# Optimization experiments

Hardware: AMD Instinct MI355X
Metric: run time of the kernel (lower is better)

The kernel has to match this reference:

```python
import jax, jax.numpy as jnp
import numpy as np

H = 128          # num_hidden
B = 512          # number of graphs (segments)
N0, N1, N2 = 500_000, 500_000, 250_000  # nodes per rank
EPS = 1e-5       # LayerNorm eps (torch default)


def setup_inputs() -> dict:
    key = jax.random.key(0)
    ks = jax.random.split(key, 24)
    s = 0.02
    inp = {
        "h0": jax.random.normal(ks[0], (N0, H), jnp.float32),
        "h1": jax.random.normal(ks[1], (N1, H), jnp.float32),
        "h2": jax.random.normal(ks[2], (N2, H), jnp.float32),
        "b0": jnp.sort(jax.random.randint(ks[3], (N0,), 0, B, jnp.int32)),
        "b1": jnp.sort(jax.random.randint(ks[4], (N1,), 0, B, jnp.int32)),
        "b2": jnp.sort(jax.random.randint(ks[5], (N2,), 0, B, jnp.int32)),
        "Wg0": jax.random.normal(ks[6], (H, 1), jnp.float32) * s,
        "bg0": jnp.zeros((1,), jnp.float32),
        "Wg1": jax.random.normal(ks[7], (H, 1), jnp.float32) * s,
        "bg1": jnp.zeros((1,), jnp.float32),
        "Wg2": jax.random.normal(ks[8], (H, 1), jnp.float32) * s,
        "bg2": jnp.zeros((1,), jnp.float32),
        "Wp0": jax.random.normal(ks[9], (4 * H, H), jnp.float32) * s,
        "bp0": jnp.zeros((H,), jnp.float32),
        "Wp1": jax.random.normal(ks[10], (4 * H, H), jnp.float32) * s,
        "bp1": jnp.zeros((H,), jnp.float32),
        "Wp2": jax.random.normal(ks[11], (4 * H, H), jnp.float32) * s,
        "bp2": jnp.zeros((H,), jnp.float32),
        "gamma": jnp.ones((3 * H,), jnp.float32),
        "beta": jnp.zeros((3 * H,), jnp.float32),
        "W1": jax.random.normal(ks[12], (3 * H, H), jnp.float32) * s,
        "b1f": jnp.zeros((H,), jnp.float32),
        "W2": jax.random.normal(ks[13], (H, 1), jnp.float32) * s,
        "b2f": jnp.zeros((1,), jnp.float32),
    }
    return inp


def _rank_vec(h, b, Wg, bg, Wp, bp):
    # gated multi-aggregation pooling over segments b -> [B, 4H] -> Linear -> [B, H]
    g = jax.nn.sigmoid(h @ Wg + bg)                      # [N, 1]
    sum_p = jax.ops.segment_sum(h, b, num_segments=B)    # [B, H]
    cnt = jax.ops.segment_sum(jnp.ones((h.shape[0], 1), h.dtype), b, num_segments=B)
    mean_p = sum_p / jnp.maximum(cnt, 1.0)
    max_p = jax.ops.segment_max(h, b, num_segments=B)
    max_p = jnp.where(cnt > 0, max_p, 0.0)               # guard empty segments
    gsum_p = jax.ops.segment_sum(g * h, b, num_segments=B)
    agg = jnp.concatenate([sum_p, mean_p, max_p, gsum_p], axis=1)  # [B, 4H]
    return agg @ Wp + bp


def reference(h0, h1, h2, b0, b1, b2,
              Wg0, bg0, Wg1, bg1, Wg2, bg2,
              Wp0, bp0, Wp1, bp1, Wp2, bp2,
              gamma, beta, W1, b1f, W2, b2f):
    r0 = _rank_vec(h0, b0, Wg0, bg0, Wp0, bp0)
    r1 = _rank_vec(h1, b1, Wg1, bg1, Wp1, bp1)
    r2 = _rank_vec(h2, b2, Wg2, bg2, Wp2, bp2)
    state = jnp.concatenate([r0, r1, r2], axis=1)        # [B, 3H]
    mu = jnp.mean(state, axis=-1, keepdims=True)
    var = jnp.mean(jnp.square(state - mu), axis=-1, keepdims=True)
    xn = (state - mu) * jax.lax.rsqrt(var + EPS) * gamma + beta
    x = jax.nn.silu(xn)
    x = jax.nn.silu(x @ W1 + b1f)
    out = x @ W2 + b2f                                   # [B, 1]
    return out[:, 0] if out.shape[-1] == 1 else out
```

## Files before the change

kernel.cpp:

```cpp
#include <hip/hip_runtime.h>
#include <hip/hip_bf16.h>
#include <math.h>

constexpr int H  = 128;
constexpr int B  = 512;
constexpr int CHUNK = 64;
constexpr int RANK_STRIDE = 3 * B * H + B;
constexpr int TOTAL_WS    = 3 * RANK_STRIDE;

__device__ __forceinline__ float atomicMaxF(float* addr, float val) {
  if (val >= 0.f) {
    return __int_as_float(atomicMax((int*)addr, __float_as_int(val)));
  } else {
    return __uint_as_float(atomicMin((unsigned int*)addr, __float_as_uint(val)));
  }
}

__global__ __launch_bounds__(256) void init_ws_kernel(float* ws) {
  int i = blockIdx.x * blockDim.x + threadIdx.x;
  if (i >= TOTAL_WS) return;
  int o = i % RANK_STRIDE;
  bool ismax = (o >= 2 * B * H) && (o < 3 * B * H);
  ws[i] = ismax ? __int_as_float(0xFF800000) : 0.0f;
}

__global__ __launch_bounds__(256) void rank_kernel(
    const float* __restrict__ h, const int* __restrict__ b,
    const float* __restrict__ Wg, const float* __restrict__ bg,
    float* __restrict__ sumb, float* __restrict__ gsumb,
    float* __restrict__ maxb, float* __restrict__ cntb, int N)
{
  const int lane = threadIdx.x & 63;
  const int wave = threadIdx.x >> 6;
  const long long gw = (long long)blockIdx.x * 4 + wave;
  const int row0 = (int)(gw * CHUNK);
  if (row0 >= N) return;
  const int row1 = min(N, row0 + CHUNK);

  const float2 wg = ((const float2*)Wg)[lane];
  const float bgv = bg[0];

  float s0 = 0.f, s1 = 0.f, g0 = 0.f, g1 = 0.f;
  float m0 = -INFINITY, m1 = -INFINITY;
  int cnt = 0;
  int cur = b[row0];

  for (int r = row0; r < row1; ++r) {
    const int seg = b[r];
    const float2 hv = ((const float2*)h)[(long long)r * 64 + lane];
    if (seg != cur) {
      const int base = cur * H + 2 * lane;
      atomicAdd(sumb + base,     s0); atomicAdd(sumb + base + 1,  s1);
      atomicAdd(gsumb + base,    g0); atomicAdd(gsumb + base + 1, g1);
      atomicMaxF(maxb + base,    m0); atomicMaxF(maxb + base + 1, m1);
      if (lane == 0) atomicAdd(cntb + cur, (float)cnt);
      s0 = s1 = g0 = g1 = 0.f; m0 = m1 = -INFINITY; cnt = 0; cur = seg;
    }
    float part = hv.x * wg.x + hv.y * wg.y;
    part += __shfl_xor(part, 1);
    part += __shfl_xor(part, 2);
    part += __shfl_xor(part, 4);
    part += __shfl_xor(part, 8);
    part += __shfl_xor(part, 16);
    part += __shfl_xor(part, 32);
    const float gate = 1.0f / (1.0f + __expf(-(part + bgv)));

    s0 += hv.x;                 s1 += hv.y;
    g0 = fmaf(gate, hv.x, g0);  g1 = fmaf(gate, hv.y, g1);
    m0 = fmaxf(m0, hv.x);       m1 = fmaxf(m1, hv.y);
    ++cnt;
  }
  if (cnt > 0) {
    const int base = cur * H + 2 * lane;
    atomicAdd(sumb + base,     s0); atomicAdd(sumb + base + 1,  s1);
    atomicAdd(gsumb + base,    g0); atomicAdd(gsumb + base + 1, g1);
    atomicMaxF(maxb + base,    m0); atomicMaxF(maxb + base + 1, m1);
    if (lane == 0) atomicAdd(cntb + cur, (float)cnt);
  }
}

__device__ __forceinline__ float siluf(float x) {
  return x / (1.0f + __expf(-x));
}

__global__ __launch_bounds__(128) void finalize_kernel(
    const float* __restrict__ ws,
    const float* __restrict__ Wp0, const float* __restrict__ bp0,
    const float* __restrict__ Wp1, const float* __restrict__ bp1,
    const float* __restrict__ Wp2, const float* __restrict__ bp2,
    const float* __restrict__ gamma, const float* __restrict__ beta,
    const float* __restrict__ W1, const float* __restrict__ b1f,
    const float* __restrict__ W2, const float* __restrict__ b2f,
    float* __restrict__ out)
{
  __shared__ float aggL[4][4 * H];
  __shared__ float state[4][3 * H];
  __shared__ float red[8];

  const int j = threadIdx.x;
  const int lane = j & 63;
  const int wv = j >> 6;
  const int gbase = blockIdx.x * 4;

  const float* Wp[3] = {Wp0, Wp1, Wp2};
  const float* bp[3] = {bp0, bp1, bp2};

  for (int k = 0; k < 3; ++k) {
    const float* sumb  = ws + k * RANK_STRIDE;
    const float* gsumb = sumb + B * H;
    const float* maxb  = sumb + 2 * B * H;
    const float* cntb  = sumb + 3 * B * H;

    for (int g = 0; g < 4; ++g) {
      const int bidx = gbase + g;
      const float c  = cntb[bidx];
      const float cm = fmaxf(c, 1.0f);
      const float sv = sumb[bidx * H + j];
      const float mv = maxb[bidx * H + j];
      const float gv = gsumb[bidx * H + j];
      aggL[g][j]         = sv;
      aggL[g][H + j]     = sv / cm;
      aggL[g][2 * H + j] = (c > 0.f) ? mv : 0.f;
      aggL[g][3 * H + j] = gv;
    }
    __syncthreads();

    const float bpv = bp[k][j];
    float r0 = bpv, r1 = bpv, r2 = bpv, r3 = bpv;
    const float* W = Wp[k];
    for (int i = 0; i < 4 * H; ++i) {
      const float w = W[i * H + j];
      r0 = fmaf(aggL[0][i], w, r0);
      r1 = fmaf(aggL[1][i], w, r1);
      r2 = fmaf(aggL[2][i], w, r2);
      r3 = fmaf(aggL[3][i], w, r3);
    }
    state[0][k * H + j] = r0;
    state[1][k * H + j] = r1;
    state[2][k * H + j] = r2;
    state[3][k * H + j] = r3;
    __syncthreads();
  }

  for (int g = 0; g < 4; ++g) {
    const float v0 = state[g][j];
    const float v1 = state[g][H + j];
    const float v2 = state[g][2 * H + j];
    float ps = v0 + v1 + v2;
    float pq = v0 * v0 + v1 * v1 + v2 * v2;
    for (int m = 1; m < 64; m <<= 1) {
      ps += __shfl_xor(ps, m);
      pq += __shfl_xor(pq, m);
    }
    if (lane == 0) { red[wv * 2] = ps; red[wv * 2 + 1] = pq; }
    __syncthreads();
    const float ts = red[0] + red[2];
    const float tq = red[1] + red[3];
    const float mu  = ts * (1.0f / 384.0f);
    const float var = tq * (1.0f / 384.0f) - mu * mu;
    const float inv = rsqrtf(var + 1e-5f);
    float x0 = (v0 - mu) * inv * gamma[j]         + beta[j];
    float x1 = (v1 - mu) * inv * gamma[H + j]     + beta[H + j];
    float x2 = (v2 - mu) * inv * gamma[2 * H + j] + beta[2 * H + j];
    state[g][j]         = siluf(x0);
    state[g][H + j]     = siluf(x1);
    state[g][2 * H + j] = siluf(x2);
    __syncthreads();
  }

  const float b1v = b1f[j];
  float a0 = b1v, a1 = b1v, a2 = b1v, a3 = b1v;
  for (int i = 0; i < 3 * H; ++i) {
    const float w = W1[i * H + j];
    a0 = fmaf(state[0][i], w, a0);
    a1 = fmaf(state[1][i], w, a1);
    a2 = fmaf(state[2][i], w, a2);
    a3 = fmaf(state[3][i], w, a3);
  }
  a0 = siluf(a0); a1 = siluf(a1); a2 = siluf(a2); a3 = siluf(a3);

  const float w2 = W2[j];
  float p0 = a0 * w2, p1 = a1 * w2, p2 = a2 * w2, p3 = a3 * w2;
  for (int m = 1; m < 64; m <<= 1) {
    p0 += __shfl_xor(p0, m);
    p1 += __shfl_xor(p1, m);
    p2 += __shfl_xor(p2, m);
    p3 += __shfl_xor(p3, m);
  }
  __syncthreads();
  if (lane == 0) {
    red[wv * 4 + 0] = p0; red[wv * 4 + 1] = p1;
    red[wv * 4 + 2] = p2; red[wv * 4 + 3] = p3;
  }
  __syncthreads();
  if (j < 4) out[gbase + j] = red[j] + red[4 + j] + b2f[0];
}

extern "C" void kernel_launch(void* const* d_in, const int* in_sizes, int n_in,
                              void* d_out, int out_size, void* d_ws, size_t ws_size,
                              hipStream_t stream) {
  const float* h0  = (const float*)d_in[0];
  const float* h1  = (const float*)d_in[1];
  const float* h2  = (const float*)d_in[2];
  const int*   b0  = (const int*)d_in[3];
  const int*   b1  = (const int*)d_in[4];
  const int*   b2  = (const int*)d_in[5];
  const float* Wg0 = (const float*)d_in[6];
  const float* bg0 = (const float*)d_in[7];
  const float* Wg1 = (const float*)d_in[8];
  const float* bg1 = (const float*)d_in[9];
  const float* Wg2 = (const float*)d_in[10];
  const float* bg2 = (const float*)d_in[11];
  const float* Wp0 = (const float*)d_in[12];
  const float* bp0 = (const float*)d_in[13];
  const float* Wp1 = (const float*)d_in[14];
  const float* bp1 = (const float*)d_in[15];
  const float* Wp2 = (const float*)d_in[16];
  const float* bp2 = (const float*)d_in[17];
  const float* gamma = (const float*)d_in[18];
  const float* beta  = (const float*)d_in[19];
  const float* W1  = (const float*)d_in[20];
  const float* b1f = (const float*)d_in[21];
  const float* W2  = (const float*)d_in[22];
  const float* b2f = (const float*)d_in[23];

  const int N0 = in_sizes[3];
  const int N1 = in_sizes[4];
  const int N2 = in_sizes[5];

  float* ws = (float*)d_ws;
  float* s0 = ws;
  float* s1 = ws + RANK_STRIDE;
  float* s2 = ws + 2 * RANK_STRIDE;

  {
    int blocks = (TOTAL_WS + 255) / 256;
    hipLaunchKernelGGL(init_ws_kernel, dim3(blocks), dim3(256), 0, stream, ws);
  }

  {
    int blocks = (N0 + 255) / 256;
    hipLaunchKernelGGL(rank_kernel, dim3(blocks), dim3(256), 0, stream,
                       h0, b0, Wg0, bg0,
                       s0, s0 + B * H, s0 + 2 * B * H, s0 + 3 * B * H, N0);
  }
  {
    int blocks = (N1 + 255) / 256;
    hipLaunchKernelGGL(rank_kernel, dim3(blocks), dim3(256), 0, stream,
                       h1, b1, Wg1, bg1,
                       s1, s1 + B * H, s1 + 2 * B * H, s1 + 3 * B * H, N1);
  }
  {
    int blocks = (N2 + 255) / 256;
    hipLaunchKernelGGL(rank_kernel, dim3(blocks), dim3(256), 0, stream,
                       h2, b2, Wg2, bg2,
                       s2, s2 + B * H, s2 + 2 * B * H, s2 + 3 * B * H, N2);
  }

  hipLaunchKernelGGL(finalize_kernel, dim3(B / 4), dim3(128), 0, stream,
                     ws, Wp0, bp0, Wp1, bp1, Wp2, bp2,
                     gamma, beta, W1, b1f, W2, b2f, (float*)d_out);
}
```

Before: 799.8 us.

## Fuse three rank pooling kernels and process two rows per wave with float4

Replaces the three per-rank reduction launches with one fused launch that picks its rank by block index. Each wave now handles 128 rows, split into two half-waves that each load a full row as float4. Segment ids are preloaded into registers and shared with shuffles. When all 64 rows in a batch belong to one segment, a fast path batches eight independent loads before reducing, which raises memory-level parallelism and cuts per-row branching and atomics. The cost is more register pressure and more complex tail and boundary handling.

```diff
diff --git a/kernel.cpp b/kernel.cpp
--- a/kernel.cpp
+++ b/kernel.cpp
@@ -4,9 +4,11 @@
 
 constexpr int H  = 128;
 constexpr int B  = 512;
-constexpr int CHUNK = 64;
 constexpr int RANK_STRIDE = 3 * B * H + B;
 constexpr int TOTAL_WS    = 3 * RANK_STRIDE;
+
+constexpr int ROWS_PER_WAVE  = 128;
+constexpr int ROWS_PER_BLOCK = 4 * ROWS_PER_WAVE;
 
 __device__ __forceinline__ float atomicMaxF(float* addr, float val) {
   if (val >= 0.f) {
@@ -24,59 +26,146 @@
   ws[i] = ismax ? __int_as_float(0xFF800000) : 0.0f;
 }
 
-__global__ __launch_bounds__(256) void rank_kernel(
-    const float* __restrict__ h, const int* __restrict__ b,
-    const float* __restrict__ Wg, const float* __restrict__ bg,
-    float* __restrict__ sumb, float* __restrict__ gsumb,
-    float* __restrict__ maxb, float* __restrict__ cntb, int N)
+__global__ __launch_bounds__(256) void rank_fused_kernel(
+    const float* __restrict__ h0, const int* __restrict__ b0,
+    const float* __restrict__ Wg0, const float* __restrict__ bg0, int N0, int nb0,
+    const float* __restrict__ h1, const int* __restrict__ b1,
+    const float* __restrict__ Wg1, const float* __restrict__ bg1, int N1, int nb1,
+    const float* __restrict__ h2, const int* __restrict__ b2,
+    const float* __restrict__ Wg2, const float* __restrict__ bg2, int N2,
+    float* __restrict__ ws)
 {
+  const int blk = blockIdx.x;
+  const float* h; const int* b; const float* Wg; const float* bg;
+  float* base; int N; int lblk;
+  if (blk < nb0) {
+    h = h0; b = b0; Wg = Wg0; bg = bg0; base = ws;                   N = N0; lblk = blk;
+  } else if (blk < nb0 + nb1) {
+    h = h1; b = b1; Wg = Wg1; bg = bg1; base = ws + RANK_STRIDE;     N = N1; lblk = blk - nb0;
+  } else {
+    h = h2; b = b2; Wg = Wg2; bg = bg2; base = ws + 2 * RANK_STRIDE; N = N2; lblk = blk - nb0 - nb1;
+  }
+
   const int lane = threadIdx.x & 63;
-  const int wave = threadIdx.x >> 6;
-  const long long gw = (long long)blockIdx.x * 4 + wave;
-  const int row0 = (int)(gw * CHUNK);
-  if (row0 >= N) return;
-  const int row1 = min(N, row0 + CHUNK);
-
-  const float2 wg = ((const float2*)Wg)[lane];
-  const float bgv = bg[0];
-
-  float s0 = 0.f, s1 = 0.f, g0 = 0.f, g1 = 0.f;
-  float m0 = -INFINITY, m1 = -INFINITY;
+  const int wv   = threadIdx.x >> 6;
+  const int half = lane >> 5;
+  const int c    = lane & 31;
+
+  const int wstart = (lblk * 4 + wv) * ROWS_PER_WAVE;
+  if (wstart >= N) return;
+  const int wend = min(wstart + ROWS_PER_WAVE, N);
+
+  float* __restrict__ sumb  = base;
+  float* __restrict__ gsumb = base + B * H;
+  float* __restrict__ maxb  = base + 2 * B * H;
+  float* __restrict__ cntb  = base + 3 * B * H;
+
+  const float4 wg  = ((const float4*)Wg)[c];
+  const float  bgv = bg[0];
+
+  const int bv0 = b[min(wstart + lane, N - 1)];
+  const int bv1 = b[min(wstart + 64 + lane, N - 1)];
+
+  float4 s  = {0.f, 0.f, 0.f, 0.f};
+  float4 gq = {0.f, 0.f, 0.f, 0.f};
+  float4 m  = {-INFINITY, -INFINITY, -INFINITY, -INFINITY};
   int cnt = 0;
-  int cur = b[row0];
-
-  for (int r = row0; r < row1; ++r) {
-    const int seg = b[r];
-    const float2 hv = ((const float2*)h)[(long long)r * 64 + lane];
-    if (seg != cur) {
-      const int base = cur * H + 2 * lane;
-      atomicAdd(sumb + base,     s0); atomicAdd(sumb + base + 1,  s1);
-      atomicAdd(gsumb + base,    g0); atomicAdd(gsumb + base + 1, g1);
-      atomicMaxF(maxb + base,    m0); atomicMaxF(maxb + base + 1, m1);
-      if (lane == 0) atomicAdd(cntb + cur, (float)cnt);
-      s0 = s1 = g0 = g1 = 0.f; m0 = m1 = -INFINITY; cnt = 0; cur = seg;
-    }
-    float part = hv.x * wg.x + hv.y * wg.y;
-    part += __shfl_xor(part, 1);
-    part += __shfl_xor(part, 2);
-    part += __shfl_xor(part, 4);
-    part += __shfl_xor(part, 8);
-    part += __shfl_xor(part, 16);
-    part += __shfl_xor(part, 32);
-    const float gate = 1.0f / (1.0f + __expf(-(part + bgv)));
-
-    s0 += hv.x;                 s1 += hv.y;
-    g0 = fmaf(gate, hv.x, g0);  g1 = fmaf(gate, hv.y, g1);
-    m0 = fmaxf(m0, hv.x);       m1 = fmaxf(m1, hv.y);
+  int cur = -1;
+
+  auto flushLane = [&]() {
+    if (cur >= 0) {
+      const int bi = cur * H + c * 4;
+      atomicAdd(sumb + bi + 0, s.x);  atomicAdd(sumb + bi + 1, s.y);
+      atomicAdd(sumb + bi + 2, s.z);  atomicAdd(sumb + bi + 3, s.w);
+      atomicAdd(gsumb + bi + 0, gq.x); atomicAdd(gsumb + bi + 1, gq.y);
+      atomicAdd(gsumb + bi + 2, gq.z); atomicAdd(gsumb + bi + 3, gq.w);
+      atomicMaxF(maxb + bi + 0, m.x); atomicMaxF(maxb + bi + 1, m.y);
+      atomicMaxF(maxb + bi + 2, m.z); atomicMaxF(maxb + bi + 3, m.w);
+      if (c == 0 && cnt) atomicAdd(cntb + cur, (float)cnt);
+      s = {0.f, 0.f, 0.f, 0.f};
+      gq = {0.f, 0.f, 0.f, 0.f};
+      m = {-INFINITY, -INFINITY, -INFINITY, -INFINITY};
+      cnt = 0;
+    }
+  };
+
+  auto gateOf = [&](float4 v) -> float {
+    float p = fmaf(v.x, wg.x, fmaf(v.y, wg.y, fmaf(v.z, wg.z, v.w * wg.w)));
+    p += __shfl_xor(p, 1);
+    p += __shfl_xor(p, 2);
+    p += __shfl_xor(p, 4);
+    p += __shfl_xor(p, 8);
+    p += __shfl_xor(p, 16);
+    return 1.0f / (1.0f + __expf(-(p + bgv)));
+  };
+
+  auto accum = [&](float4 v, float gt) {
+    s.x += v.x; s.y += v.y; s.z += v.z; s.w += v.w;
+    gq.x = fmaf(gt, v.x, gq.x); gq.y = fmaf(gt, v.y, gq.y);
+    gq.z = fmaf(gt, v.z, gq.z); gq.w = fmaf(gt, v.w, gq.w);
+    m.x = fmaxf(m.x, v.x); m.y = fmaxf(m.y, v.y);
+    m.z = fmaxf(m.z, v.z); m.w = fmaxf(m.w, v.w);
+  };
+
+  const float4* __restrict__ hp = (const float4*)h;
+
+  int r = wstart;
+  while (r + 64 <= wend) {
+    const int bv = (r - wstart < 64) ? bv0 : bv1;
+    const int sA = __shfl(bv, 0);
+    const int sB = __shfl(bv, 63);
+    if (sA == sB) {
+      if (sA != cur) { flushLane(); cur = sA; }
+      #pragma unroll
+      for (int g = 0; g < 4; ++g) {
+        float4 v[8];
+        #pragma unroll
+        for (int i = 0; i < 8; ++i)
+          v[i] = hp[(size_t)(r + g * 16 + 2 * i + half) * 32 + c];
+        #pragma unroll
+        for (int i = 0; i < 8; ++i) {
+          const float gt = gateOf(v[i]);
+          accum(v[i], gt);
+        }
+      }
+      cnt += 32;
+    } else {
+      #pragma unroll 4
+      for (int i = 0; i < 32; ++i) {
+        const int seg = __shfl(bv, 2 * i + half);
+        const float4 v = hp[(size_t)(r + 2 * i + half) * 32 + c];
+        const float gt = gateOf(v);
+        if (seg != cur) { flushLane(); cur = seg; }
+        accum(v, gt);
+        ++cnt;
+      }
+    }
+    r += 64;
+  }
+  while (r + 2 <= wend) {
+    const int o = r - wstart;
+    const int bv = (o < 64) ? bv0 : bv1;
+    const int seg = __shfl(bv, (o & 63) + half);
+    const float4 v = hp[(size_t)(r + half) * 32 + c];
+    const float gt = gateOf(v);
+    if (seg != cur) { flushLane(); cur = seg; }
+    accum(v, gt);
     ++cnt;
-  }
-  if (cnt > 0) {
-    const int base = cur * H + 2 * lane;
-    atomicAdd(sumb + base,     s0); atomicAdd(sumb + base + 1,  s1);
-    atomicAdd(gsumb + base,    g0); atomicAdd(gsumb + base + 1, g1);
-    atomicMaxF(maxb + base,    m0); atomicMaxF(maxb + base + 1, m1);
-    if (lane == 0) atomicAdd(cntb + cur, (float)cnt);
-  }
+    r += 2;
+  }
+  if (r < wend) {
+    const int o = r - wstart;
+    const int bv = (o < 64) ? bv0 : bv1;
+    const int seg = __shfl(bv, o & 63);
+    const float4 v = hp[(size_t)r * 32 + c];
+    const float gt = gateOf(v);
+    if (half == 0) {
+      if (seg != cur) { flushLane(); cur = seg; }
+      accum(v, gt);
+      ++cnt;
+    }
+  }
+  flushLane();
 }
 
 __device__ __forceinline__ float siluf(float x) {
@@ -113,14 +202,14 @@
 
     for (int g = 0; g < 4; ++g) {
       const int bidx = gbase + g;
-      const float c  = cntb[bidx];
-      const float cm = fmaxf(c, 1.0f);
+      const float cc = cntb[bidx];
+      const float cm = fmaxf(cc, 1.0f);
       const float sv = sumb[bidx * H + j];
       const float mv = maxb[bidx * H + j];
       const float gv = gsumb[bidx * H + j];
       aggL[g][j]         = sv;
       aggL[g][H + j]     = sv / cm;
-      aggL[g][2 * H + j] = (c > 0.f) ? mv : 0.f;
+      aggL[g][2 * H + j] = (cc > 0.f) ? mv : 0.f;
       aggL[g][3 * H + j] = gv;
     }
     __syncthreads();
@@ -148,9 +237,9 @@
     const float v2 = state[g][2 * H + j];
     float ps = v0 + v1 + v2;
     float pq = v0 * v0 + v1 * v1 + v2 * v2;
-    for (int m = 1; m < 64; m <<= 1) {
-      ps += __shfl_xor(ps, m);
-      pq += __shfl_xor(pq, m);
+    for (int mm = 1; mm < 64; mm <<= 1) {
+      ps += __shfl_xor(ps, mm);
+      pq += __shfl_xor(pq, mm);
     }
     if (lane == 0) { red[wv * 2] = ps; red[wv * 2 + 1] = pq; }
     __syncthreads();
@@ -181,11 +270,11 @@
 
   const float w2 = W2[j];
   float p0 = a0 * w2, p1 = a1 * w2, p2 = a2 * w2, p3 = a3 * w2;
-  for (int m = 1; m < 64; m <<= 1) {
-    p0 += __shfl_xor(p0, m);
-    p1 += __shfl_xor(p1, m);
-    p2 += __shfl_xor(p2, m);
-    p3 += __shfl_xor(p3, m);
+  for (int mm = 1; mm < 64; mm <<= 1) {
+    p0 += __shfl_xor(p0, mm);
+    p1 += __shfl_xor(p1, mm);
+    p2 += __shfl_xor(p2, mm);
+    p3 += __shfl_xor(p3, mm);
   }
   __syncthreads();
   if (lane == 0) {
@@ -229,33 +318,20 @@
   const int N2 = in_sizes[5];
 
   float* ws = (float*)d_ws;
-  float* s0 = ws;
-  float* s1 = ws + RANK_STRIDE;
-  float* s2 = ws + 2 * RANK_STRIDE;
 
   {
     int blocks = (TOTAL_WS + 255) / 256;
     hipLaunchKernelGGL(init_ws_kernel, dim3(blocks), dim3(256), 0, stream, ws);
   }
 
-  {
-    int blocks = (N0 + 255) / 256;
-    hipLaunchKernelGGL(rank_kernel, dim3(blocks), dim3(256), 0, stream,
-                       h0, b0, Wg0, bg0,
-                       s0, s0 + B * H, s0 + 2 * B * H, s0 + 3 * B * H, N0);
-  }
-  {
-    int blocks = (N1 + 255) / 256;
-    hipLaunchKernelGGL(rank_kernel, dim3(blocks), dim3(256), 0, stream,
-                       h1, b1, Wg1, bg1,
-                       s1, s1 + B * H, s1 + 2 * B * H, s1 + 3 * B * H, N1);
-  }
-  {
-    int blocks = (N2 + 255) / 256;
-    hipLaunchKernelGGL(rank_kernel, dim3(blocks), dim3(256), 0, stream,
-                       h2, b2, Wg2, bg2,
-                       s2, s2 + B * H, s2 + 2 * B * H, s2 + 3 * B * H, N2);
-  }
+  const int nb0 = (N0 + ROWS_PER_BLOCK - 1) / ROWS_PER_BLOCK;
+  const int nb1 = (N1 + ROWS_PER_BLOCK - 1) / ROWS_PER_BLOCK;
+  const int nb2 = (N2 + ROWS_PER_BLOCK - 1) / ROWS_PER_BLOCK;
+  hipLaunchKernelGGL(rank_fused_kernel, dim3(nb0 + nb1 + nb2), dim3(256), 0, stream,
+                     h0, b0, Wg0, bg0, N0, nb0,
+                     h1, b1, Wg1, bg1, N1, nb1,
+                     h2, b2, Wg2, bg2, N2,
+                     ws);
 
   hipLaunchKernelGGL(finalize_kernel, dim3(B / 4), dim3(128), 0, stream,
                      ws, Wp0, bp0, Wp1, bp1, Wp2, bp2,
```

Measured after the change: 790.4 us. No clear change (-1.2%).
